# Performance work log

Measured on AMD Instinct MI355X. Metric: run time of the kernel, lower is better.

Reference implementation:

```python
import jax, jax.numpy as jnp
import numpy as np

N_NODES = 50000


def gcn_conv(x, W, b, src, dst, n_nodes):
    """PyG-style GCNConv: out = D^{-1/2} (A + I) D^{-1/2} (x W) + b."""
    xw = x @ W  # [N, out_dim]
    loop = jnp.arange(n_nodes, dtype=src.dtype)
    src_f = jnp.concatenate([src, loop])  # edges + self-loops
    dst_f = jnp.concatenate([dst, loop])
    deg = jax.ops.segment_sum(jnp.ones_like(dst_f, dtype=xw.dtype), dst_f,
                              num_segments=n_nodes)
    dinv = jnp.where(deg > 0, jax.lax.rsqrt(deg), 0.0)
    norm = dinv[src_f] * dinv[dst_f]  # [E+N]
    msgs = xw[src_f] * norm[:, None]  # gather + scale
    out = jax.ops.segment_sum(msgs, dst_f, num_segments=n_nodes)
    return out + b


def setup_inputs() -> dict:
    key = jax.random.key(0)
    ks = jax.random.split(key, 8)
    n, e = N_NODES, 800000
    in_d, hid, out_d = 128, 256, 64
    x = jax.random.normal(ks[0], (n, in_d), dtype=jnp.float32)
    edge_index = jax.random.randint(ks[1], (2, e), 0, n, dtype=jnp.int32)
    sc = lambda f: 1.0 / np.sqrt(f)
    W1 = jax.random.normal(ks[2], (in_d, hid), dtype=jnp.float32) * sc(in_d)
    b1 = jnp.zeros((hid,), jnp.float32)
    W2 = jax.random.normal(ks[3], (hid, hid), dtype=jnp.float32) * sc(hid)
    b2 = jnp.zeros((hid,), jnp.float32)
    W_final = jax.random.normal(ks[4], (hid, out_d), dtype=jnp.float32) * sc(hid)
    b_final = jnp.zeros((out_d,), jnp.float32)
    W_skip = jax.random.normal(ks[5], (in_d, out_d), dtype=jnp.float32) * sc(in_d)
    b_skip = jnp.zeros((out_d,), jnp.float32)
    return {"x": x, "edge_index": edge_index, "W1": W1, "b1": b1,
            "W2": W2, "b2": b2, "W_final": W_final, "b_final": b_final,
            "W_skip": W_skip, "b_skip": b_skip}


def reference(x, edge_index, W1, b1, W2, b2, W_final, b_final, W_skip, b_skip):
    n = x.shape[0]
    src, dst = edge_index[0], edge_index[1]
    h = jax.nn.relu(gcn_conv(x, W1, b1, src, dst, n))
    h = jax.nn.relu(gcn_conv(h, W2, b2, src, dst, n))
    return h @ W_final + b_final + (x @ W_skip + b_skip)
```

## Files before the change

kernel.cpp:

```cpp
#include <hip/hip_runtime.h>

#define N_NODES 50000
#define N_EDGES 800000
#define HB 782

typedef float f32x4 __attribute__((ext_vector_type(4)));
typedef float f32x2 __attribute__((ext_vector_type(2)));
typedef __bf16 bf16x8 __attribute__((ext_vector_type(8)));
typedef __bf16 bf16x4 __attribute__((ext_vector_type(4)));


__global__ void zero_deg(int4* __restrict__ p, int n4) {
    int i = blockIdx.x * blockDim.x + threadIdx.x;
    if (i < n4) p[i] = make_int4(0, 0, 0, 0);
}

#define CAST_N4 (N_NODES * 32)
#define PREP_ITEMS (CAST_N4 + 32768 + 65536 + 16384 + 8192 + 64)
#define PREP_BLOCKS ((PREP_ITEMS + 255) / 256)

__global__ void mega_prep(const int* __restrict__ dst, int* __restrict__ deg,
                          int* __restrict__ rank,
                          const float* __restrict__ x, __bf16* __restrict__ x_bf,
                          const float* __restrict__ W1, const float* __restrict__ W2,
                          const float* __restrict__ Wf, const float* __restrict__ Ws,
                          const float* __restrict__ bfb, const float* __restrict__ bsb,
                          __bf16* __restrict__ W1t, __bf16* __restrict__ W2t,
                          __bf16* __restrict__ Wft, __bf16* __restrict__ Wst,
                          float* __restrict__ bfinal) {
    int b = blockIdx.x;
    if (b < HB) {
        int i = (b * 256 + threadIdx.x) * 4;
        if (i >= N_EDGES) return;
        int4 d = *(const int4*)(dst + i);
        int4 r;
        r.x = atomicAdd(&deg[d.x], 1);
        r.y = atomicAdd(&deg[d.y], 1);
        r.z = atomicAdd(&deg[d.z], 1);
        r.w = atomicAdd(&deg[d.w], 1);
        *(int4*)(rank + i) = r;
        return;
    }
    int idx = (b - HB) * 256 + threadIdx.x;
    if (idx < CAST_N4) {
        float4 v = ((const float4*)x)[idx];
        bf16x4 a = {(__bf16)v.x, (__bf16)v.y, (__bf16)v.z, (__bf16)v.w};
        __builtin_nontemporal_store(a, (bf16x4*)x_bf + idx);
        return;
    }
    int j = idx - CAST_N4;
    if (j < 32768) {
        int n = j >> 7, k = j & 127;
        W1t[j] = (__bf16)W1[k * 256 + n];
    } else if (j < 32768 + 65536) {
        int i = j - 32768;
        int n = i >> 8, k = i & 255;
        W2t[i] = (__bf16)W2[k * 256 + n];
    } else if (j < 32768 + 65536 + 16384) {
        int i = j - (32768 + 65536);
        int n = i >> 8, k = i & 255;
        Wft[i] = (__bf16)Wf[k * 64 + n];
    } else if (j < 32768 + 65536 + 16384 + 8192) {
        int i = j - (32768 + 65536 + 16384);
        int n = i >> 7, k = i & 127;
        Wst[i] = (__bf16)Ws[k * 64 + n];
    } else if (j < 32768 + 65536 + 16384 + 8192 + 64) {
        int i = j - (32768 + 65536 + 16384 + 8192);
        bfinal[i] = bfb[i] + bsb[i];
    }
}

__device__ __forceinline__ int wave_incl_scan(int x) {
    int lane = threadIdx.x & 63;
#pragma unroll
    for (int off = 1; off < 64; off <<= 1) {
        int y = __shfl_up(x, off, 64);
        if (lane >= off) x += y;
    }
    return x;
}

__global__ void scan_partial_dinv(const int* __restrict__ in, int n,
                                  int* __restrict__ out_partial, int* __restrict__ blocksum,
                                  float* __restrict__ dinv) {
    __shared__ int wsum[8];
    int i = blockIdx.x * 512 + threadIdx.x;
    int v = (i < n) ? in[i] : 0;
    if (i < n) dinv[i] = rsqrtf((float)(v + 1));
    int inc = wave_incl_scan(v);
    int lane = threadIdx.x & 63, wid = threadIdx.x >> 6;
    if (lane == 63) wsum[wid] = inc;
    __syncthreads();
    if (wid == 0) {
        int w = (lane < 8) ? wsum[lane] : 0;
        int wi = wave_incl_scan(w);
        if (lane < 8) wsum[lane] = wi;
    }
    __syncthreads();
    int woff = (wid == 0) ? 0 : wsum[wid - 1];
    if (i < n) out_partial[i] = woff + inc - v;
    if (threadIdx.x == 0) blocksum[blockIdx.x] = wsum[7];
}

__global__ void scan_add_fused(int* __restrict__ rowptr, int n,
                               const int* __restrict__ blocksum, int nb, int total) {
    __shared__ int sexc[128];
    __shared__ int w0tot;
    int t = threadIdx.x;
    if (t < 128) {
        int v = (t < nb) ? blocksum[t] : 0;
        int inc = wave_incl_scan(v);
        sexc[t] = inc - v;
        if (t == 63) w0tot = inc;
    }
    __syncthreads();
    int b = blockIdx.x;
    int boff = sexc[b] + (b >= 64 ? w0tot : 0);
    int i = b * 512 + t;
    if (i < n) rowptr[i] += boff;
    if (i == 0) rowptr[n] = total;
}

#define XS_ITEMS (N_NODES * 16)
#define XS_BLOCKS ((XS_ITEMS + 255) / 256)

__global__ void fill_xs(const int* __restrict__ src, const int* __restrict__ dst,
                        const int* __restrict__ rank,
                        const int* __restrict__ rowptr, int* __restrict__ csr_src,
                        const __bf16* __restrict__ x_bf, const float* __restrict__ dinv,
                        __bf16* __restrict__ x_s) {
    int b = blockIdx.x;
    if (b < HB) {
        int i = (b * 256 + threadIdx.x) * 4;
        if (i >= N_EDGES) return;
        int4 d = *(const int4*)(dst + i);
        int4 s = *(const int4*)(src + i);
        int4 r = *(const int4*)(rank + i);
        csr_src[rowptr[d.x] + r.x] = s.x;
        csr_src[rowptr[d.y] + r.y] = s.y;
        csr_src[rowptr[d.z] + r.z] = s.z;
        csr_src[rowptr[d.w] + r.w] = s.w;
        return;
    }
    int j = (b - HB) * 256 + threadIdx.x;
    if (j < XS_ITEMS) {
        bf16x8 v = ((const bf16x8*)x_bf)[j];
        float di = dinv[j >> 4];
        bf16x8 o;
#pragma unroll
        for (int k = 0; k < 8; ++k) o[k] = (__bf16)(di * (float)v[k]);
        ((bf16x8*)x_s)[j] = o;
    }
}


template <int V> struct VecSel;
template <> struct VecSel<4> { using T = bf16x4; };
template <> struct VecSel<8> { using T = bf16x8; };

template <int F>
__global__ __launch_bounds__(256) void aggregate_half(const __bf16* __restrict__ in_s, __bf16* __restrict__ out,
                                                      const int* __restrict__ rowptr, const int* __restrict__ csr_src,
                                                      const float* __restrict__ dinv) {
    constexpr int VB = F / 32;
    using VT = typename VecSel<VB>::T;
    int node = blockIdx.x * 4 + (threadIdx.x >> 6);
    int lane = threadIdx.x & 63;
    int lh = lane & 31;
    int half = lane >> 5;
    const __bf16* colbase = in_s + (size_t)lh * VB;

    float acc[VB] = {};
    if (half == 0) {
        VT v = *(const VT*)(colbase + (size_t)node * F);
#pragma unroll
        for (int j = 0; j < VB; ++j) acc[j] = (float)v[j];
    }

    int beg = rowptr[node], end = rowptr[node + 1];
    int e = beg;
    for (; e + 16 <= end; e += 16) {
        int ss[8];
#pragma unroll
        for (int k = 0; k < 8; ++k) ss[k] = csr_src[e + 2 * k + half];
        VT v[8];
#pragma unroll
        for (int k = 0; k < 8; ++k) v[k] = *(const VT*)(colbase + (size_t)ss[k] * F);
#pragma unroll
        for (int k = 0; k < 8; ++k)
#pragma unroll
            for (int j = 0; j < VB; ++j) acc[j] += (float)v[k][j];
    }
    for (; e + 8 <= end; e += 8) {
        int s0 = csr_src[e + half], s1 = csr_src[e + 2 + half];
        int s2 = csr_src[e + 4 + half], s3 = csr_src[e + 6 + half];
        VT v0 = *(const VT*)(colbase + (size_t)s0 * F);
        VT v1 = *(const VT*)(colbase + (size_t)s1 * F);
        VT v2 = *(const VT*)(colbase + (size_t)s2 * F);
        VT v3 = *(const VT*)(colbase + (size_t)s3 * F);
#pragma unroll
        for (int j = 0; j < VB; ++j) {
            acc[j] += (float)v0[j];
            acc[j] += (float)v1[j];
            acc[j] += (float)v2[j];
            acc[j] += (float)v3[j];
        }
    }
    for (; e + 2 <= end; e += 2) {
        int s = csr_src[e + half];
        VT v = *(const VT*)(colbase + (size_t)s * F);
#pragma unroll
        for (int j = 0; j < VB; ++j) acc[j] += (float)v[j];
    }
    if (e < end && half == 0) {
        int s = csr_src[e];
        VT v = *(const VT*)(colbase + (size_t)s * F);
#pragma unroll
        for (int j = 0; j < VB; ++j) acc[j] += (float)v[j];
    }

    float di = dinv[node];
    VT o;
#pragma unroll
    for (int j = 0; j < VB; ++j) {
        float t = acc[j] + __shfl_xor(acc[j], 32);
        o[j] = (__bf16)(di * t);
    }
    if (half == 0) __builtin_nontemporal_store(o, (VT*)(out + (size_t)node * F + lh * VB));
}


__global__ __launch_bounds__(256) void aggregate_fp8(const unsigned char* __restrict__ in_s, __bf16* __restrict__ out,
                                                     const int* __restrict__ rowptr, const int* __restrict__ csr_src,
                                                     const float* __restrict__ dinv) {
    constexpr int F = 256;
    int node = blockIdx.x * 4 + (threadIdx.x >> 6);
    int lane = threadIdx.x & 63;
    int lh = lane & 31;
    int half = lane >> 5;
    const unsigned char* colbase = in_s + lh * 8;

    float acc[8] = {};
    auto decode_acc = [&](uint2 v) {
        f32x2 p0 = __builtin_amdgcn_cvt_pk_f32_fp8(v.x, false);
        f32x2 p1 = __builtin_amdgcn_cvt_pk_f32_fp8(v.x, true);
        f32x2 p2 = __builtin_amdgcn_cvt_pk_f32_fp8(v.y, false);
        f32x2 p3 = __builtin_amdgcn_cvt_pk_f32_fp8(v.y, true);
        acc[0] += p0[0]; acc[1] += p0[1]; acc[2] += p1[0]; acc[3] += p1[1];
        acc[4] += p2[0]; acc[5] += p2[1]; acc[6] += p3[0]; acc[7] += p3[1];
    };

    if (half == 0) decode_acc(*(const uint2*)(colbase + (size_t)node * F));

    int beg = rowptr[node], end = rowptr[node + 1];
    int e = beg;
    for (; e + 16 <= end; e += 16) {
        int ss[8];
#pragma unroll
        for (int k = 0; k < 8; ++k) ss[k] = csr_src[e + 2 * k + half];
        uint2 v[8];
#pragma unroll
        for (int k = 0; k < 8; ++k) v[k] = *(const uint2*)(colbase + (size_t)ss[k] * F);
#pragma unroll
        for (int k = 0; k < 8; ++k) decode_acc(v[k]);
    }
    for (; e + 8 <= end; e += 8) {
        int s0 = csr_src[e + half], s1 = csr_src[e + 2 + half];
        int s2 = csr_src[e + 4 + half], s3 = csr_src[e + 6 + half];
        uint2 v0 = *(const uint2*)(colbase + (size_t)s0 * F);
        uint2 v1 = *(const uint2*)(colbase + (size_t)s1 * F);
        uint2 v2 = *(const uint2*)(colbase + (size_t)s2 * F);
        uint2 v3 = *(const uint2*)(colbase + (size_t)s3 * F);
        decode_acc(v0); decode_acc(v1); decode_acc(v2); decode_acc(v3);
    }
    for (; e + 2 <= end; e += 2) {
        int s = csr_src[e + half];
        decode_acc(*(const uint2*)(colbase + (size_t)s * F));
    }
    if (e < end && half == 0) decode_acc(*(const uint2*)(colbase + (size_t)csr_src[e] * F));

    float di = dinv[node];
    bf16x8 o;
#pragma unroll
    for (int j = 0; j < 8; ++j) {
        float t = acc[j] + __shfl_xor(acc[j], 32);
        o[j] = (__bf16)(di * t);
    }
    if (half == 0) __builtin_nontemporal_store(o, (bf16x8*)(out + (size_t)node * F + lh * 8));
}


template <int NROWS, int NTH>
__device__ __forceinline__ void stage_tile(const __bf16* __restrict__ src, int K, int row0, int rowclamp,
                                           int k0, char* lds) {
    int t = threadIdx.x;
#pragma unroll
    for (int p = 0; p < NROWS * 8 / NTH; ++p) {
        int G = p * NTH + t;
        int r = G >> 3, gp = G & 7;
        int g = gp ^ (r & 7);
        int gr = row0 + r;
        if (gr > rowclamp) gr = rowclamp;
        const __bf16* sp = src + (size_t)gr * K + k0 + g * 8;
        __builtin_amdgcn_global_load_lds((const __attribute__((address_space(1))) void*)sp,
                                         (__attribute__((address_space(3))) void*)(lds + G * 16), 16, 0, 0);
    }
}


template <bool SCALE, bool OUT_FP8>
__global__ __launch_bounds__(512, 4) void mfma_gemm_wide(const __bf16* __restrict__ A, const __bf16* __restrict__ Bt,
                                                         int K, const float* __restrict__ bias,
                                                         const float* __restrict__ dinv,
                                                         void* __restrict__ Cout, int M) {
    constexpr int N = 256;
    __shared__ alignas(16) char lds[81920];
    const int lane = threadIdx.x & 63, wid = threadIdx.x >> 6;
    const int row0 = blockIdx.x * 64;
    const int kg = lane >> 4, l15 = lane & 15;

    f32x4 acc[4][2];
#pragma unroll
    for (int mi = 0; mi < 4; ++mi)
#pragma unroll
        for (int ni = 0; ni < 2; ++ni) acc[mi][ni] = {0.f, 0.f, 0.f, 0.f};

    auto STAGE = [&](int buf, int k0) {
        char* base = lds + buf * 40960;
        stage_tile<64, 512>(A, K, row0, M - 1, k0, base);
        stage_tile<256, 512>(Bt, K, 0, N - 1, k0, base + 8192);
    };

    const int nt = K >> 6;
    STAGE(0, 0);
    __syncthreads();
    int cur = 0;
    for (int t = 0; t < nt; ++t) {
        if (t + 1 < nt) STAGE(cur ^ 1, (t + 1) * 64);
        char* As = lds + cur * 40960;
        char* Bs = As + 8192;
        bf16x8 af[4][2], bfr[2][2];
#pragma unroll
        for (int mi = 0; mi < 4; ++mi) {
            int r = mi * 16 + l15;
#pragma unroll
            for (int kf = 0; kf < 2; ++kf) {
                int slot = (kf * 4 + kg) ^ (r & 7);
                af[mi][kf] = *(const bf16x8*)(As + r * 128 + slot * 16);
            }
        }
#pragma unroll
        for (int ni = 0; ni < 2; ++ni) {
            int r = wid * 32 + ni * 16 + l15;
#pragma unroll
            for (int kf = 0; kf < 2; ++kf) {
                int slot = (kf * 4 + kg) ^ (r & 7);
                bfr[ni][kf] = *(const bf16x8*)(Bs + r * 128 + slot * 16);
            }
        }
#pragma unroll
        for (int mi = 0; mi < 4; ++mi)
#pragma unroll
            for (int ni = 0; ni < 2; ++ni)
#pragma unroll
                for (int kf = 0; kf < 2; ++kf)
                    acc[mi][ni] = __builtin_amdgcn_mfma_f32_16x16x32_bf16(af[mi][kf], bfr[ni][kf],
                                                                          acc[mi][ni], 0, 0, 0);
        __syncthreads();
        cur ^= 1;
    }

#pragma unroll
    for (int mi = 0; mi < 4; ++mi) {
#pragma unroll
        for (int q = 0; q < 4; ++q) {
            int gr = row0 + mi * 16 + kg * 4 + q;
            if (gr >= M) continue;
            float sc = SCALE ? dinv[gr] : 1.0f;
            int col0 = wid * 32 + l15;
            float v0 = fmaxf(acc[mi][0][q] + bias[col0], 0.f);
            float v1 = fmaxf(acc[mi][1][q] + bias[col0 + 16], 0.f);
            if (SCALE) { v0 *= sc; v1 *= sc; }
            if constexpr (OUT_FP8) {
                int w = __builtin_amdgcn_cvt_pk_fp8_f32(v0, v1, 0, false);
                unsigned char* Cp = (unsigned char*)Cout + (size_t)gr * N;
                Cp[col0] = (unsigned char)(w & 0xff);
                Cp[col0 + 16] = (unsigned char)((w >> 8) & 0xff);
            } else {
                __bf16* Cp = (__bf16*)Cout + (size_t)gr * N;
                Cp[col0] = (__bf16)v0;
                Cp[col0 + 16] = (__bf16)v1;
            }
        }
    }
}


__global__ __launch_bounds__(256, 4) void mfma_gemm_final(const __bf16* __restrict__ A1, const __bf16* __restrict__ B1t, int K1,
                                                          const __bf16* __restrict__ A2, const __bf16* __restrict__ B2t, int K2,
                                                          const float* __restrict__ bias, float* __restrict__ Cout, int M) {
    constexpr int N = 64;
    __shared__ alignas(16) char lds[32768];
    const int lane = threadIdx.x & 63, wid = threadIdx.x >> 6;
    const int wm = wid >> 1, wn = wid & 1;
    const int row0 = blockIdx.x * 64;
    const int kg = lane >> 4, l15 = lane & 15;

    f32x4 acc[2][2];
#pragma unroll
    for (int mi = 0; mi < 2; ++mi)
#pragma unroll
        for (int ni = 0; ni < 2; ++ni) acc[mi][ni] = {0.f, 0.f, 0.f, 0.f};

    const int nt1 = K1 >> 6, nt = nt1 + (K2 >> 6);
    auto STAGE = [&](int buf, int tile) {
        const __bf16* A = (tile < nt1) ? A1 : A2;
        const __bf16* Bt = (tile < nt1) ? B1t : B2t;
        int K = (tile < nt1) ? K1 : K2;
        int k0 = ((tile < nt1) ? tile : tile - nt1) * 64;
        char* base = lds + buf * 16384;
        stage_tile<64, 256>(A, K, row0, M - 1, k0, base);
        stage_tile<64, 256>(Bt, K, 0, N - 1, k0, base + 8192);
    };

    STAGE(0, 0);
    __syncthreads();
    int cur = 0;
    for (int t = 0; t < nt; ++t) {
        if (t + 1 < nt) STAGE(cur ^ 1, t + 1);
        char* As = lds + cur * 16384;
        char* Bs = As + 8192;
        bf16x8 af[2][2], bfr[2][2];
#pragma unroll
        for (int mi = 0; mi < 2; ++mi) {
            int r = wm * 32 + mi * 16 + l15;
#pragma unroll
            for (int kf = 0; kf < 2; ++kf) {
                int slot = (kf * 4 + kg) ^ (r & 7);
                af[mi][kf] = *(const bf16x8*)(As + r * 128 + slot * 16);
            }
        }
#pragma unroll
        for (int ni = 0; ni < 2; ++ni) {
            int r = wn * 32 + ni * 16 + l15;
#pragma unroll
            for (int kf = 0; kf < 2; ++kf) {
                int slot = (kf * 4 + kg) ^ (r & 7);
                bfr[ni][kf] = *(const bf16x8*)(Bs + r * 128 + slot * 16);
            }
        }
#pragma unroll
        for (int mi = 0; mi < 2; ++mi)
#pragma unroll
            for (int ni = 0; ni < 2; ++ni)
#pragma unroll
                for (int kf = 0; kf < 2; ++kf)
                    acc[mi][ni] = __builtin_amdgcn_mfma_f32_16x16x32_bf16(af[mi][kf], bfr[ni][kf],
                                                                          acc[mi][ni], 0, 0, 0);
        __syncthreads();
        cur ^= 1;
    }

#pragma unroll
    for (int mi = 0; mi < 2; ++mi) {
#pragma unroll
        for (int ni = 0; ni < 2; ++ni) {
            int col = wn * 32 + ni * 16 + l15;
            float bv = bias[col];
#pragma unroll
            for (int q = 0; q < 4; ++q) {
                int gr = row0 + wm * 32 + mi * 16 + kg * 4 + q;
                if (gr < M) Cout[(size_t)gr * N + col] = acc[mi][ni][q] + bv;
            }
        }
    }
}


extern "C" void kernel_launch(void* const* d_in, const int* in_sizes, int n_in,
                              void* d_out, int out_size, void* d_ws, size_t ws_size,
                              hipStream_t stream) {
    const float* x  = (const float*)d_in[0];
    const int*   ei = (const int*)d_in[1];
    const int*   src = ei;
    const int*   dst = ei + N_EDGES;
    const float* W1 = (const float*)d_in[2];
    const float* b1 = (const float*)d_in[3];
    const float* W2 = (const float*)d_in[4];
    const float* b2 = (const float*)d_in[5];
    const float* Wf = (const float*)d_in[6];
    const float* bf = (const float*)d_in[7];
    const float* Ws = (const float*)d_in[8];
    const float* bs = (const float*)d_in[9];
    float* out = (float*)d_out;

    char* ws = (char*)d_ws;
    size_t off = 0;
    auto alloc = [&](size_t bytes) -> void* {
        void* p = ws + off;
        off += (bytes + 255) & ~(size_t)255;
        return p;
    };
    int*           deg      = (int*)alloc(N_NODES * 4);
    int*           rank     = (int*)alloc(N_EDGES * 4);
    int*           rowptr   = (int*)alloc((N_NODES + 1) * 4);
    float*         dinv     = (float*)alloc(N_NODES * 4);
    int*           blocksum = (int*)alloc(4096);
    int*           csr      = (int*)alloc(N_EDGES * 4);
    __bf16*        x_bf     = (__bf16*)alloc((size_t)N_NODES * 128 * 2);
    __bf16*        x_s      = (__bf16*)alloc((size_t)N_NODES * 128 * 2);
    __bf16*        W1t      = (__bf16*)alloc(128 * 256 * 2);
    __bf16*        W2t      = (__bf16*)alloc(256 * 256 * 2);
    __bf16*        Wft      = (__bf16*)alloc(256 * 64 * 2);
    __bf16*        Wst      = (__bf16*)alloc(128 * 64 * 2);
    float*         bfinal   = (float*)alloc(64 * 4);
    __bf16*        bufP1    = (__bf16*)alloc((size_t)N_NODES * 256 * 2);
    unsigned char* bufP2    = (unsigned char*)alloc((size_t)N_NODES * 256);
    __bf16*        bufP3    = (__bf16*)alloc((size_t)N_NODES * 256 * 2);

    zero_deg<<<(N_NODES / 4 + 255) / 256, 256, 0, stream>>>((int4*)deg, N_NODES / 4);

    mega_prep<<<HB + PREP_BLOCKS, 256, 0, stream>>>(dst, deg, rank, x, x_bf,
                                                    W1, W2, Wf, Ws, bf, bs,
                                                    W1t, W2t, Wft, Wst, bfinal);

    int nb = (N_NODES + 511) / 512;
    scan_partial_dinv<<<nb, 512, 0, stream>>>(deg, N_NODES, rowptr, blocksum, dinv);
    scan_add_fused<<<nb, 512, 0, stream>>>(rowptr, N_NODES, blocksum, nb, N_EDGES);

    fill_xs<<<HB + XS_BLOCKS, 256, 0, stream>>>(src, dst, rank, rowptr, csr, x_bf, dinv, x_s);

    const int gm64 = (N_NODES + 63) / 64;

    aggregate_half<128><<<(N_NODES + 3) / 4, 256, 0, stream>>>(x_s, bufP1, rowptr, csr, dinv);
    mfma_gemm_wide<true, true><<<gm64, 512, 0, stream>>>(bufP1, W1t, 128, b1, dinv, bufP2, N_NODES);

    aggregate_fp8<<<(N_NODES + 3) / 4, 256, 0, stream>>>(bufP2, bufP3, rowptr, csr, dinv);
    mfma_gemm_wide<false, false><<<gm64, 512, 0, stream>>>(bufP3, W2t, 256, b2, nullptr, bufP1, N_NODES);

    mfma_gemm_final<<<gm64, 256, 0, stream>>>(bufP1, Wft, 256, x_bf, Wst, 128, bfinal, out, N_NODES);
}
```

Baseline: 193.3 us.

## Replace global-atomic degree count with per-block LDS histograms over node ranges

Degree counting and rank assignment now run in 192 blocks, each owning a slice of 261 nodes. Each block scans the whole dst array and does atomics in shared memory, then writes its degree slice directly, so the separate zero_deg launch goes away. This removes global atomic contention and one kernel launch. In exchange every histogram block reads all 800K dst indices (about 3.2 MB each), adding heavy redundant L2 traffic, and prep blocks grow to 512 threads.

```diff
diff --git a/kernel.cpp b/kernel.cpp
--- a/kernel.cpp
+++ b/kernel.cpp
@@ -2,46 +2,53 @@
 
 #define N_NODES 50000
 #define N_EDGES 800000
-#define HB 782
+#define NB_HIST 192
+#define NPB 261
+#define E4 (N_EDGES / 4)
 
 typedef float f32x4 __attribute__((ext_vector_type(4)));
 typedef float f32x2 __attribute__((ext_vector_type(2)));
 typedef __bf16 bf16x8 __attribute__((ext_vector_type(8)));
 typedef __bf16 bf16x4 __attribute__((ext_vector_type(4)));
 
-
-__global__ void zero_deg(int4* __restrict__ p, int n4) {
-    int i = blockIdx.x * blockDim.x + threadIdx.x;
-    if (i < n4) p[i] = make_int4(0, 0, 0, 0);
-}
-
 #define CAST_N4 (N_NODES * 32)
 #define PREP_ITEMS (CAST_N4 + 32768 + 65536 + 16384 + 8192 + 64)
-#define PREP_BLOCKS ((PREP_ITEMS + 255) / 256)
-
-__global__ void mega_prep(const int* __restrict__ dst, int* __restrict__ deg,
-                          int* __restrict__ rank,
-                          const float* __restrict__ x, __bf16* __restrict__ x_bf,
-                          const float* __restrict__ W1, const float* __restrict__ W2,
-                          const float* __restrict__ Wf, const float* __restrict__ Ws,
-                          const float* __restrict__ bfb, const float* __restrict__ bsb,
-                          __bf16* __restrict__ W1t, __bf16* __restrict__ W2t,
-                          __bf16* __restrict__ Wft, __bf16* __restrict__ Wst,
-                          float* __restrict__ bfinal) {
+#define PREP_BLOCKS ((PREP_ITEMS + 511) / 512)
+
+__global__ __launch_bounds__(512) void hist_prep(const int* __restrict__ dst, int* __restrict__ deg,
+                                                 int* __restrict__ rank,
+                                                 const float* __restrict__ x, __bf16* __restrict__ x_bf,
+                                                 const float* __restrict__ W1, const float* __restrict__ W2,
+                                                 const float* __restrict__ Wf, const float* __restrict__ Ws,
+                                                 const float* __restrict__ bfb, const float* __restrict__ bsb,
+                                                 __bf16* __restrict__ W1t, __bf16* __restrict__ W2t,
+                                                 __bf16* __restrict__ Wft, __bf16* __restrict__ Wst,
+                                                 float* __restrict__ bfinal) {
     int b = blockIdx.x;
-    if (b < HB) {
-        int i = (b * 256 + threadIdx.x) * 4;
-        if (i >= N_EDGES) return;
-        int4 d = *(const int4*)(dst + i);
-        int4 r;
-        r.x = atomicAdd(&deg[d.x], 1);
-        r.y = atomicAdd(&deg[d.y], 1);
-        r.z = atomicAdd(&deg[d.z], 1);
-        r.w = atomicAdd(&deg[d.w], 1);
-        *(int4*)(rank + i) = r;
+    if (b < NB_HIST) {
+        __shared__ int h[NPB];
+        const int base = b * NPB;
+        const unsigned count = (unsigned)min(NPB, N_NODES - base);
+        for (int i = threadIdx.x; i < NPB; i += 512) h[i] = 0;
+        __syncthreads();
+        const int4* d4 = (const int4*)dst;
+        for (int i = threadIdx.x; i < E4; i += 512) {
+            int4 d = d4[i];
+            int e = i * 4;
+            unsigned r0 = (unsigned)(d.x - base);
+            unsigned r1 = (unsigned)(d.y - base);
+            unsigned r2 = (unsigned)(d.z - base);
+            unsigned r3 = (unsigned)(d.w - base);
+            if (r0 < count) rank[e + 0] = atomicAdd(&h[r0], 1);
+            if (r1 < count) rank[e + 1] = atomicAdd(&h[r1], 1);
+            if (r2 < count) rank[e + 2] = atomicAdd(&h[r2], 1);
+            if (r3 < count) rank[e + 3] = atomicAdd(&h[r3], 1);
+        }
+        __syncthreads();
+        for (int i = threadIdx.x; i < (int)count; i += 512) deg[base + i] = h[i];
         return;
     }
-    int idx = (b - HB) * 256 + threadIdx.x;
+    int idx = (b - NB_HIST) * 512 + threadIdx.x;
     if (idx < CAST_N4) {
         float4 v = ((const float4*)x)[idx];
         bf16x4 a = {(__bf16)v.x, (__bf16)v.y, (__bf16)v.z, (__bf16)v.w};
@@ -121,6 +128,7 @@
     if (i == 0) rowptr[n] = total;
 }
 
+#define HB 782
 #define XS_ITEMS (N_NODES * 16)
 #define XS_BLOCKS ((XS_ITEMS + 255) / 256)
 
@@ -518,11 +526,9 @@
     unsigned char* bufP2    = (unsigned char*)alloc((size_t)N_NODES * 256);
     __bf16*        bufP3    = (__bf16*)alloc((size_t)N_NODES * 256 * 2);
 
-    zero_deg<<<(N_NODES / 4 + 255) / 256, 256, 0, stream>>>((int4*)deg, N_NODES / 4);
-
-    mega_prep<<<HB + PREP_BLOCKS, 256, 0, stream>>>(dst, deg, rank, x, x_bf,
-                                                    W1, W2, Wf, Ws, bf, bs,
-                                                    W1t, W2t, Wft, Wst, bfinal);
+    hist_prep<<<NB_HIST + PREP_BLOCKS, 512, 0, stream>>>(dst, deg, rank, x, x_bf,
+                                                         W1, W2, Wf, Ws, bf, bs,
+                                                         W1t, W2t, Wft, Wst, bfinal);
 
     int nb = (N_NODES + 511) / 512;
     scan_partial_dinv<<<nb, 512, 0, stream>>>(deg, N_NODES, rowptr, blocksum, dinv);
```

Result: slower. 290.6 us (+50.4%).
